# Kernel tuning notes

Hardware: AMD Instinct MI355X
Metric: run time of the kernel (lower is better)

The kernel has to match this reference:

```python
import jax, jax.numpy as jnp
import numpy as np

D_MODEL = 2048
N_HEADS = 16
D_HEAD = D_MODEL // N_HEADS  # 128
WINDOW = 512
SCALE = D_HEAD ** -0.5


def setup_inputs() -> dict:
    key = jax.random.key(0)
    ks = jax.random.split(key, 5)
    B, S = 2, 4096
    x = jax.random.normal(ks[0], (B, S, D_MODEL), dtype=jnp.float32)
    W_qkv = jax.random.normal(ks[1], (D_MODEL, 3 * D_MODEL), dtype=jnp.float32) * (D_MODEL ** -0.5)
    b_qkv = jax.random.normal(ks[2], (3 * D_MODEL,), dtype=jnp.float32) * 0.02
    W_out = jax.random.normal(ks[3], (D_MODEL, D_MODEL), dtype=jnp.float32) * (D_MODEL ** -0.5)
    b_out = jax.random.normal(ks[4], (D_MODEL,), dtype=jnp.float32) * 0.02
    return {"x": x, "W_qkv": W_qkv, "b_qkv": b_qkv, "W_out": W_out, "b_out": b_out}


def reference(x, W_qkv, b_qkv, W_out, b_out):
    B, S, D = x.shape
    nb = S // WINDOW  # number of independent causal windows (block-diagonal attention)
    qkv = x @ W_qkv + b_qkv  # (B,S,3D)
    q, k, v = jnp.split(qkv, 3, axis=-1)

    def to_blocks(t):
        # (B,S,D) -> (B,H,nb,W,dh)
        return t.reshape(B, nb, WINDOW, N_HEADS, D_HEAD).transpose(0, 3, 1, 2, 4)

    q, k, v = to_blocks(q), to_blocks(k), to_blocks(v)
    # per-window attention scores: (B,H,nb,W,W)
    scores = jnp.einsum('bhnqd,bhnkd->bhnqk', q, k) * SCALE
    causal = jnp.tril(jnp.ones((WINDOW, WINDOW), dtype=bool))
    scores = jnp.where(causal, scores, -jnp.inf)
    attn = jax.nn.softmax(scores, axis=-1)
    out = jnp.einsum('bhnqk,bhnkd->bhnqd', attn, v)  # (B,H,nb,W,dh)
    out = out.transpose(0, 2, 3, 1, 4).reshape(B, S, D)
    return out @ W_out + b_out
```

## Files before the change

kernel.cpp:

```cpp
#include <hip/hip_runtime.h>
#include <stdint.h>


typedef unsigned short u16;
typedef unsigned int u32;
typedef __attribute__((ext_vector_type(8))) short bf16x8;
typedef __attribute__((ext_vector_type(4))) float f32x4;

#define QKVN 6144
#define DM 2048

__device__ __forceinline__ u16 f2b(float f) {
  u32 u = __builtin_bit_cast(u32, f);
  u32 r = (u + 0x7fffu + ((u >> 16) & 1u)) >> 16;
  return (u16)r;
}

__device__ __forceinline__ void gload_lds16(const void* g, void* l) {
  __builtin_amdgcn_global_load_lds((const __attribute__((address_space(1))) void*)g,
                                   (__attribute__((address_space(3))) void*)l,
                                   16, 0, 0);
}


__global__ void cast_f32_bf16(const float4* __restrict__ x, uint4* __restrict__ o) {
  int idx = blockIdx.x * 256 + threadIdx.x;
  float4 a = x[2 * idx];
  float4 b = x[2 * idx + 1];
  uint4 r;
  r.x = (u32)f2b(a.x) | ((u32)f2b(a.y) << 16);
  r.y = (u32)f2b(a.z) | ((u32)f2b(a.w) << 16);
  r.z = (u32)f2b(b.x) | ((u32)f2b(b.y) << 16);
  r.w = (u32)f2b(b.z) | ((u32)f2b(b.w) << 16);
  o[idx] = r;
}

__global__ void transpose_cast(const float* __restrict__ W, u16* __restrict__ Wt,
                               int K, int N) {
  __shared__ u16 tile[64][65];
  int tx = threadIdx.x & 63;
  int ty = threadIdx.x >> 6;
  int n0 = blockIdx.x * 64;
  int k0 = blockIdx.y * 64;
#pragma unroll
  for (int r = 0; r < 64; r += 4)
    tile[r + ty][tx] = f2b(W[(size_t)(k0 + r + ty) * N + n0 + tx]);
  __syncthreads();
#pragma unroll
  for (int r = 0; r < 64; r += 4)
    Wt[(size_t)(n0 + r + ty) * K + k0 + tx] = tile[tx][r + ty];
}


template <typename TO>
__global__ __launch_bounds__(256, 3) void gemm_bt(const u16* __restrict__ A,
                                                  const u16* __restrict__ Bt,
                                                  const float* __restrict__ bias,
                                                  TO* __restrict__ C,
                                                  int M, int N, int K) {
  __shared__ u16 As[128 * 64];
  __shared__ u16 Bs[128 * 64];
  const int tid = threadIdx.x;
  const int lane = tid & 63;
  const int wave = tid >> 6;
  const int quad = lane >> 4;
  const int l15 = lane & 15;
  const int m0 = blockIdx.y * 128;
  const int n0 = blockIdx.x * 128;
  const int wm = (wave & 1) * 64;
  const int wn = (wave >> 1) * 64;

  f32x4 acc[4][4] = {};

  for (int k0 = 0; k0 < K; k0 += 64) {
#pragma unroll
    for (int i = 0; i < 4; ++i) {
      int sb = wave * 256 + i * 64;
      int s = sb + lane;
      int m = s >> 3;
      int c = (s & 7) ^ (m & 7);
      gload_lds16(A + (size_t)(m0 + m) * K + (k0 + c * 8), As + sb * 8);
      gload_lds16(Bt + (size_t)(n0 + m) * K + (k0 + c * 8), Bs + sb * 8);
    }
    __syncthreads();
#pragma unroll
    for (int ks = 0; ks < 2; ++ks) {
      bf16x8 af[4], bf[4];
#pragma unroll
      for (int i = 0; i < 4; ++i) {
        int m = wm + i * 16 + l15;
        af[i] = *(const bf16x8*)(As + m * 64 + (((ks * 4 + quad) ^ (m & 7)) << 3));
        int n = wn + i * 16 + l15;
        bf[i] = *(const bf16x8*)(Bs + n * 64 + (((ks * 4 + quad) ^ (n & 7)) << 3));
      }
#pragma unroll
      for (int i = 0; i < 4; ++i)
#pragma unroll
        for (int j = 0; j < 4; ++j)
          acc[i][j] = __builtin_amdgcn_mfma_f32_16x16x32_bf16(af[i], bf[j], acc[i][j], 0, 0, 0);
    }
    __syncthreads();
  }

#pragma unroll
  for (int j = 0; j < 4; ++j) {
    int col = n0 + wn + j * 16 + l15;
    float bv = bias[col];
#pragma unroll
    for (int i = 0; i < 4; ++i) {
      int row = m0 + wm + i * 16 + quad * 4;
#pragma unroll
      for (int t = 0; t < 4; ++t) {
        float v = acc[i][j][t] + bv;
        if constexpr (sizeof(TO) == 2)
          C[(size_t)(row + t) * N + col] = (TO)f2b(v);
        else
          C[(size_t)(row + t) * N + col] = (TO)v;
      }
    }
  }
}


__global__ __launch_bounds__(256, 2) void attn_win(const u16* __restrict__ qkv,
                                                   u16* __restrict__ attn_out) {
  __shared__ u16 Vt[128 * 64];
  __shared__ u16 Ps[128 * 64];
  const int tid = threadIdx.x;
  const int lane = tid & 63;
  const int wave = tid >> 6;
  const int quad = lane >> 4;
  const int l15 = lane & 15;
  const int qt = blockIdx.x;
  const int win = blockIdx.y;
  const int b = blockIdx.z >> 4;
  const int h = blockIdx.z & 15;
  const int tokw = b * 4096 + win * 512;
  const int tokq = tokw + qt * 128;
  const float SCALE = 0.08838834764831845f;

  bf16x8 qf[2][4];
  {
    const u16* Qb = qkv + (size_t)tokq * QKVN + h * 128;
#pragma unroll
    for (int j = 0; j < 2; ++j) {
      const u16* Qr = Qb + (size_t)(wave * 32 + j * 16 + l15) * QKVN + quad * 8;
#pragma unroll
      for (int ks = 0; ks < 4; ++ks)
        qf[j][ks] = *(const bf16x8*)(Qr + ks * 32);
    }
  }

  f32x4 acc_o[8][2] = {};
  float mrun[2] = {-1e30f, -1e30f};
  float lrun[2] = {0.f, 0.f};

  const int jt_end = 2 * qt + 1;
  for (int jt = 0; jt <= jt_end; ++jt) {
    {
      const u16* Vb = qkv + (size_t)(tokw + jt * 64) * QKVN + 4096 + h * 128;
#pragma unroll
      for (int it = 0; it < 2; ++it) {
        int task = it * 256 + tid;
        int p = task & 31;
        int dc = task >> 5;
        int kk0 = p * 2;
        const u16* g0 = Vb + (size_t)kk0 * QKVN + dc * 8;
        uint4 r0 = *(const uint4*)g0;
        uint4 r1 = *(const uint4*)(g0 + QKVN);
        const u16* a0 = (const u16*)&r0;
        const u16* a1 = (const u16*)&r1;
        int c = kk0 >> 3;
        int boff = (kk0 & 7) << 1;
#pragma unroll
        for (int j = 0; j < 8; ++j) {
          int d = dc * 8 + j;
          *(u32*)((char*)Vt + d * 128 + ((c ^ (d & 7)) << 4) + boff) =
              (u32)a0[j] | ((u32)a1[j] << 16);
        }
      }
    }

    f32x4 acc_s[4][2] = {};
    {
      const u16* Kb = qkv + (size_t)(tokw + jt * 64) * QKVN + 2048 + h * 128;
      bf16x8 kf[4][4];
#pragma unroll
      for (int i = 0; i < 4; ++i) {
        const u16* Kr = Kb + (size_t)(i * 16 + l15) * QKVN + quad * 8;
#pragma unroll
        for (int ks = 0; ks < 4; ++ks)
          kf[i][ks] = *(const bf16x8*)(Kr + ks * 32);
      }
#pragma unroll
      for (int ks = 0; ks < 4; ++ks)
#pragma unroll
        for (int i = 0; i < 4; ++i)
#pragma unroll
          for (int j = 0; j < 2; ++j)
            acc_s[i][j] = __builtin_amdgcn_mfma_f32_16x16x32_bf16(kf[i][ks], qf[j][ks],
                                                                  acc_s[i][j], 0, 0, 0);
    }

    const bool need_mask = (jt >= 2 * qt);
#pragma unroll
    for (int j = 0; j < 2; ++j) {
      int ql = wave * 32 + j * 16 + l15;
      int qg = qt * 128 + ql;
      float vmax = -1e30f;
#pragma unroll
      for (int i = 0; i < 4; ++i)
#pragma unroll
        for (int t = 0; t < 4; ++t) {
          float s = acc_s[i][j][t] * SCALE;
          if (need_mask) {
            int kg = jt * 64 + i * 16 + quad * 4 + t;
            if (kg > qg) s = -1e30f;
          }
          acc_s[i][j][t] = s;
          vmax = fmaxf(vmax, s);
        }
      vmax = fmaxf(vmax, __shfl_xor(vmax, 16));
      vmax = fmaxf(vmax, __shfl_xor(vmax, 32));
      float mnew = fmaxf(mrun[j], vmax);
      float alpha = __expf(mrun[j] - mnew);
      mrun[j] = mnew;
      float vsum = 0.f;
#pragma unroll
      for (int i = 0; i < 4; ++i) {
        float p0 = __expf(acc_s[i][j][0] - mnew);
        float p1 = __expf(acc_s[i][j][1] - mnew);
        float p2 = __expf(acc_s[i][j][2] - mnew);
        float p3 = __expf(acc_s[i][j][3] - mnew);
        vsum += (p0 + p1) + (p2 + p3);
        uint2 pk;
        pk.x = (u32)f2b(p0) | ((u32)f2b(p1) << 16);
        pk.y = (u32)f2b(p2) | ((u32)f2b(p3) << 16);
        int kk = i * 16 + quad * 4;
        *(uint2*)((char*)Ps + ql * 128 + (((kk >> 3) ^ (ql & 7)) << 4) + ((kk & 7) << 1)) = pk;
      }
      vsum += __shfl_xor(vsum, 16);
      vsum += __shfl_xor(vsum, 32);
      lrun[j] = lrun[j] * alpha + vsum;
#pragma unroll
      for (int i2 = 0; i2 < 8; ++i2)
#pragma unroll
        for (int t = 0; t < 4; ++t)
          acc_o[i2][j][t] *= alpha;
    }
    __syncthreads();

#pragma unroll
    for (int ks = 0; ks < 2; ++ks) {
      int kk = ks * 32 + quad * 8;
      int kc = kk >> 3;
      bf16x8 pf[2];
#pragma unroll
      for (int j = 0; j < 2; ++j) {
        int ql = wave * 32 + j * 16 + l15;
        pf[j] = *(const bf16x8*)((char*)Ps + ql * 128 + ((kc ^ (ql & 7)) << 4));
      }
#pragma unroll
      for (int i2 = 0; i2 < 8; ++i2) {
        int d = i2 * 16 + l15;
        bf16x8 vf = *(const bf16x8*)((char*)Vt + d * 128 + ((kc ^ (d & 7)) << 4));
#pragma unroll
        for (int j = 0; j < 2; ++j)
          acc_o[i2][j] = __builtin_amdgcn_mfma_f32_16x16x32_bf16(vf, pf[j], acc_o[i2][j], 0, 0, 0);
      }
    }
    __syncthreads();
  }

#pragma unroll
  for (int j = 0; j < 2; ++j) {
    float inv = 1.0f / lrun[j];
    int ql = wave * 32 + j * 16 + l15;
    u16* orow = attn_out + (size_t)(tokq + ql) * DM + h * 128;
#pragma unroll
    for (int i2 = 0; i2 < 8; ++i2) {
      int d = i2 * 16 + quad * 4;
      uint2 pk;
      pk.x = (u32)f2b(acc_o[i2][j][0] * inv) | ((u32)f2b(acc_o[i2][j][1] * inv) << 16);
      pk.y = (u32)f2b(acc_o[i2][j][2] * inv) | ((u32)f2b(acc_o[i2][j][3] * inv) << 16);
      *(uint2*)(orow + d) = pk;
    }
  }
}


extern "C" void kernel_launch(void* const* d_in, const int* in_sizes, int n_in,
                              void* d_out, int out_size, void* d_ws, size_t ws_size,
                              hipStream_t stream) {
  const float* x = (const float*)d_in[0];
  const float* W_qkv = (const float*)d_in[1];
  const float* b_qkv = (const float*)d_in[2];
  const float* W_out = (const float*)d_in[3];
  const float* b_out = (const float*)d_in[4];
  float* out = (float*)d_out;

  char* w = (char*)d_ws;
  u16* xb = (u16*)w;
  u16* wqkvT = (u16*)(w + 33554432);
  u16* woutT = (u16*)(w + 33554432 + 25165824);
  u16* qkv = (u16*)(w + 67108864);

  cast_f32_bf16<<<8192, 256, 0, stream>>>((const float4*)x, (uint4*)xb);
  transpose_cast<<<dim3(96, 32), 256, 0, stream>>>(W_qkv, wqkvT, 2048, 6144);
  transpose_cast<<<dim3(32, 32), 256, 0, stream>>>(W_out, woutT, 2048, 2048);
  gemm_bt<u16><<<dim3(48, 64), 256, 0, stream>>>(xb, wqkvT, b_qkv, qkv, 8192, 6144, 2048);
  attn_win<<<dim3(4, 8, 32), 256, 0, stream>>>(qkv, xb);
  gemm_bt<float><<<dim3(16, 64), 256, 0, stream>>>(xb, woutT, b_out, out, 8192, 2048, 2048);
}
```

Baseline: 523.8 us.

## Widen GEMM tiles, double-buffer attention LDS, use exp2 softmax with fast packing

GEMM blocks now compute 128x256 tiles with 8 accumulator columns per wave, reducing redundant A loads and block count; occupancy is lowered to 2 blocks. Attention double-buffers V and P in LDS, which drops the second barrier per step. It prefetches V before the QK MFMAs, splits masked and unmasked iterations via a template, folds the scale into exp2, and skips the output rescale when alpha is near 1. The bf16 packing of probabilities now truncates instead of rounding, slightly changing numerics.

```diff
diff --git a/kernel.cpp b/kernel.cpp
--- a/kernel.cpp
+++ b/kernel.cpp
@@ -15,6 +15,13 @@
   u32 r = (u + 0x7fffu + ((u >> 16) & 1u)) >> 16;
   return (u16)r;
 }
+
+__device__ __forceinline__ u32 pack_hi16(float hi, float lo) {
+  return __builtin_amdgcn_perm(__builtin_bit_cast(u32, hi),
+                               __builtin_bit_cast(u32, lo), 0x07060302u);
+}
+
+__device__ __forceinline__ float fexp2(float x) { return __builtin_amdgcn_exp2f(x); }
 
 __device__ __forceinline__ void gload_lds16(const void* g, void* l) {
   __builtin_amdgcn_global_load_lds((const __attribute__((address_space(1))) void*)g,
@@ -53,24 +60,24 @@
 
 
 template <typename TO>
-__global__ __launch_bounds__(256, 3) void gemm_bt(const u16* __restrict__ A,
+__global__ __launch_bounds__(256, 2) void gemm_bt(const u16* __restrict__ A,
                                                   const u16* __restrict__ Bt,
                                                   const float* __restrict__ bias,
                                                   TO* __restrict__ C,
                                                   int M, int N, int K) {
   __shared__ u16 As[128 * 64];
-  __shared__ u16 Bs[128 * 64];
+  __shared__ u16 Bs[256 * 64];
   const int tid = threadIdx.x;
   const int lane = tid & 63;
   const int wave = tid >> 6;
   const int quad = lane >> 4;
   const int l15 = lane & 15;
   const int m0 = blockIdx.y * 128;
-  const int n0 = blockIdx.x * 128;
+  const int n0 = blockIdx.x * 256;
   const int wm = (wave & 1) * 64;
-  const int wn = (wave >> 1) * 64;
-
-  f32x4 acc[4][4] = {};
+  const int wn = (wave >> 1) * 128;
+
+  f32x4 acc[4][8] = {};
 
   for (int k0 = 0; k0 < K; k0 += 64) {
 #pragma unroll
@@ -80,30 +87,40 @@
       int m = s >> 3;
       int c = (s & 7) ^ (m & 7);
       gload_lds16(A + (size_t)(m0 + m) * K + (k0 + c * 8), As + sb * 8);
-      gload_lds16(Bt + (size_t)(n0 + m) * K + (k0 + c * 8), Bs + sb * 8);
+    }
+#pragma unroll
+    for (int i = 0; i < 8; ++i) {
+      int sb = wave * 512 + i * 64;
+      int s = sb + lane;
+      int n = s >> 3;
+      int c = (s & 7) ^ (n & 7);
+      gload_lds16(Bt + (size_t)(n0 + n) * K + (k0 + c * 8), Bs + sb * 8);
     }
     __syncthreads();
 #pragma unroll
     for (int ks = 0; ks < 2; ++ks) {
-      bf16x8 af[4], bf[4];
+      bf16x8 af[4], bf[8];
 #pragma unroll
       for (int i = 0; i < 4; ++i) {
         int m = wm + i * 16 + l15;
         af[i] = *(const bf16x8*)(As + m * 64 + (((ks * 4 + quad) ^ (m & 7)) << 3));
-        int n = wn + i * 16 + l15;
-        bf[i] = *(const bf16x8*)(Bs + n * 64 + (((ks * 4 + quad) ^ (n & 7)) << 3));
       }
 #pragma unroll
+      for (int j = 0; j < 8; ++j) {
+        int n = wn + j * 16 + l15;
+        bf[j] = *(const bf16x8*)(Bs + n * 64 + (((ks * 4 + quad) ^ (n & 7)) << 3));
+      }
+#pragma unroll
       for (int i = 0; i < 4; ++i)
 #pragma unroll
-        for (int j = 0; j < 4; ++j)
+        for (int j = 0; j < 8; ++j)
           acc[i][j] = __builtin_amdgcn_mfma_f32_16x16x32_bf16(af[i], bf[j], acc[i][j], 0, 0, 0);
     }
     __syncthreads();
   }
 
 #pragma unroll
-  for (int j = 0; j < 4; ++j) {
+  for (int j = 0; j < 8; ++j) {
     int col = n0 + wn + j * 16 + l15;
     float bv = bias[col];
 #pragma unroll
@@ -122,10 +139,137 @@
 }
 
 
+template <bool MASK>
+__device__ __forceinline__ void attn_step(
+    int jt, int tid, int wave, int quad, int l15, int qt, int tokw, int h,
+    const u16* __restrict__ qkv, u16* Vt, u16* Ps,
+    const bf16x8 (&qf)[2][4], f32x4 (&acc_o)[8][2], float (&mrun)[2],
+    float (&lrun)[2]) {
+  const float SL2E = 0.12751745f;
+  u16* VtB = Vt + (jt & 1) * (128 * 64);
+  u16* PsB = Ps + (jt & 1) * (128 * 64);
+
+  const u16* Vb = qkv + (size_t)(tokw + jt * 64) * QKVN + 4096 + h * 128;
+  const int p = tid & 31;
+  const int dc0 = tid >> 5;
+  const int kk0 = p * 2;
+  const u16* g0 = Vb + (size_t)kk0 * QKVN + dc0 * 8;
+  uint4 vr0 = *(const uint4*)g0;
+  uint4 vr1 = *(const uint4*)(g0 + QKVN);
+  uint4 vr2 = *(const uint4*)(g0 + 64);
+  uint4 vr3 = *(const uint4*)(g0 + QKVN + 64);
+
+  f32x4 acc_s[4][2] = {};
+  {
+    const u16* Kb = qkv + (size_t)(tokw + jt * 64) * QKVN + 2048 + h * 128;
+    bf16x8 kf[4][4];
+#pragma unroll
+    for (int i = 0; i < 4; ++i) {
+      const u16* Kr = Kb + (size_t)(i * 16 + l15) * QKVN + quad * 8;
+#pragma unroll
+      for (int ks = 0; ks < 4; ++ks)
+        kf[i][ks] = *(const bf16x8*)(Kr + ks * 32);
+    }
+#pragma unroll
+    for (int ks = 0; ks < 4; ++ks)
+#pragma unroll
+      for (int i = 0; i < 4; ++i)
+#pragma unroll
+        for (int j = 0; j < 2; ++j)
+          acc_s[i][j] = __builtin_amdgcn_mfma_f32_16x16x32_bf16(kf[i][ks], qf[j][ks],
+                                                                acc_s[i][j], 0, 0, 0);
+  }
+
+  {
+    const u16* a0 = (const u16*)&vr0;
+    const u16* a1 = (const u16*)&vr1;
+    const u16* a2 = (const u16*)&vr2;
+    const u16* a3 = (const u16*)&vr3;
+    int c = kk0 >> 3;
+    int boff = (kk0 & 7) << 1;
+#pragma unroll
+    for (int j = 0; j < 8; ++j) {
+      int d = dc0 * 8 + j;
+      *(u32*)((char*)VtB + d * 128 + ((c ^ (d & 7)) << 4) + boff) =
+          (u32)a0[j] | ((u32)a1[j] << 16);
+      int d2 = d + 64;
+      *(u32*)((char*)VtB + d2 * 128 + ((c ^ (d2 & 7)) << 4) + boff) =
+          (u32)a2[j] | ((u32)a3[j] << 16);
+    }
+  }
+
+#pragma unroll
+  for (int j = 0; j < 2; ++j) {
+    int ql = wave * 32 + j * 16 + l15;
+    float vmax = -1e30f;
+#pragma unroll
+    for (int i = 0; i < 4; ++i)
+#pragma unroll
+      for (int t = 0; t < 4; ++t) {
+        float s = acc_s[i][j][t];
+        if (MASK) {
+          int kg = jt * 64 + i * 16 + quad * 4 + t;
+          if (kg > qt * 128 + ql) s = -1e30f;
+          acc_s[i][j][t] = s;
+        }
+        vmax = fmaxf(vmax, s);
+      }
+    vmax = fmaxf(vmax, __shfl_xor(vmax, 16));
+    vmax = fmaxf(vmax, __shfl_xor(vmax, 32));
+    float mnew = fmaxf(mrun[j], vmax * SL2E);
+    float alpha = fexp2(mrun[j] - mnew);
+    mrun[j] = mnew;
+    float vsum = 0.f;
+#pragma unroll
+    for (int i = 0; i < 4; ++i) {
+      float p0 = fexp2(__builtin_fmaf(acc_s[i][j][0], SL2E, -mnew));
+      float p1 = fexp2(__builtin_fmaf(acc_s[i][j][1], SL2E, -mnew));
+      float p2 = fexp2(__builtin_fmaf(acc_s[i][j][2], SL2E, -mnew));
+      float p3 = fexp2(__builtin_fmaf(acc_s[i][j][3], SL2E, -mnew));
+      vsum += (p0 + p1) + (p2 + p3);
+      uint2 pk;
+      pk.x = pack_hi16(p1, p0);
+      pk.y = pack_hi16(p3, p2);
+      int kk = i * 16 + quad * 4;
+      *(uint2*)((char*)PsB + ql * 128 + (((kk >> 3) ^ (ql & 7)) << 4) + ((kk & 7) << 1)) = pk;
+    }
+    vsum += __shfl_xor(vsum, 16);
+    vsum += __shfl_xor(vsum, 32);
+    lrun[j] = lrun[j] * alpha + vsum;
+    if (__ballot(alpha < 0.99995f)) {
+#pragma unroll
+      for (int i2 = 0; i2 < 8; ++i2)
+#pragma unroll
+        for (int t = 0; t < 4; ++t)
+          acc_o[i2][j][t] *= alpha;
+    }
+  }
+  __syncthreads();
+
+#pragma unroll
+  for (int ks = 0; ks < 2; ++ks) {
+    int kc = ks * 4 + quad;
+    bf16x8 pf[2];
+#pragma unroll
+    for (int j = 0; j < 2; ++j) {
+      int ql = wave * 32 + j * 16 + l15;
+      pf[j] = *(const bf16x8*)((char*)PsB + ql * 128 + ((kc ^ (ql & 7)) << 4));
+    }
+#pragma unroll
+    for (int i2 = 0; i2 < 8; ++i2) {
+      int d = i2 * 16 + l15;
+      bf16x8 vf = *(const bf16x8*)((char*)VtB + d * 128 + ((kc ^ (d & 7)) << 4));
+#pragma unroll
+      for (int j = 0; j < 2; ++j)
+        acc_o[i2][j] = __builtin_amdgcn_mfma_f32_16x16x32_bf16(vf, pf[j], acc_o[i2][j], 0, 0, 0);
+    }
+  }
+}
+
 __global__ __launch_bounds__(256, 2) void attn_win(const u16* __restrict__ qkv,
                                                    u16* __restrict__ attn_out) {
-  __shared__ u16 Vt[128 * 64];
-  __shared__ u16 Ps[128 * 64];
+  __shared__ u16 Vt[2 * 128 * 64];
+  __shared__ u16 Ps[2 * 128 * 64];
   const int tid = threadIdx.x;
   const int lane = tid & 63;
   const int wave = tid >> 6;
@@ -137,7 +281,6 @@
   const int h = blockIdx.z & 15;
   const int tokw = b * 4096 + win * 512;
   const int tokq = tokw + qt * 128;
-  const float SCALE = 0.08838834764831845f;
 
   bf16x8 qf[2][4];
   {
@@ -155,122 +298,12 @@
   float mrun[2] = {-1e30f, -1e30f};
   float lrun[2] = {0.f, 0.f};
 
-  const int jt_end = 2 * qt + 1;
-  for (int jt = 0; jt <= jt_end; ++jt) {
-    {
-      const u16* Vb = qkv + (size_t)(tokw + jt * 64) * QKVN + 4096 + h * 128;
-#pragma unroll
-      for (int it = 0; it < 2; ++it) {
-        int task = it * 256 + tid;
-        int p = task & 31;
-        int dc = task >> 5;
-        int kk0 = p * 2;
-        const u16* g0 = Vb + (size_t)kk0 * QKVN + dc * 8;
-        uint4 r0 = *(const uint4*)g0;
-        uint4 r1 = *(const uint4*)(g0 + QKVN);
-        const u16* a0 = (const u16*)&r0;
-        const u16* a1 = (const u16*)&r1;
-        int c = kk0 >> 3;
-        int boff = (kk0 & 7) << 1;
-#pragma unroll
-        for (int j = 0; j < 8; ++j) {
-          int d = dc * 8 + j;
-          *(u32*)((char*)Vt + d * 128 + ((c ^ (d & 7)) << 4) + boff) =
-              (u32)a0[j] | ((u32)a1[j] << 16);
-        }
-      }
-    }
-
-    f32x4 acc_s[4][2] = {};
-    {
-      const u16* Kb = qkv + (size_t)(tokw + jt * 64) * QKVN + 2048 + h * 128;
-      bf16x8 kf[4][4];
-#pragma unroll
-      for (int i = 0; i < 4; ++i) {
-        const u16* Kr = Kb + (size_t)(i * 16 + l15) * QKVN + quad * 8;
-#pragma unroll
-        for (int ks = 0; ks < 4; ++ks)
-          kf[i][ks] = *(const bf16x8*)(Kr + ks * 32);
-      }
-#pragma unroll
-      for (int ks = 0; ks < 4; ++ks)
-#pragma unroll
-        for (int i = 0; i < 4; ++i)
-#pragma unroll
-          for (int j = 0; j < 2; ++j)
-            acc_s[i][j] = __builtin_amdgcn_mfma_f32_16x16x32_bf16(kf[i][ks], qf[j][ks],
-                                                                  acc_s[i][j], 0, 0, 0);
-    }
-
-    const bool need_mask = (jt >= 2 * qt);
-#pragma unroll
-    for (int j = 0; j < 2; ++j) {
-      int ql = wave * 32 + j * 16 + l15;
-      int qg = qt * 128 + ql;
-      float vmax = -1e30f;
-#pragma unroll
-      for (int i = 0; i < 4; ++i)
-#pragma unroll
-        for (int t = 0; t < 4; ++t) {
-          float s = acc_s[i][j][t] * SCALE;
-          if (need_mask) {
-            int kg = jt * 64 + i * 16 + quad * 4 + t;
-            if (kg > qg) s = -1e30f;
-          }
-          acc_s[i][j][t] = s;
-          vmax = fmaxf(vmax, s);
-        }
-      vmax = fmaxf(vmax, __shfl_xor(vmax, 16));
-      vmax = fmaxf(vmax, __shfl_xor(vmax, 32));
-      float mnew = fmaxf(mrun[j], vmax);
-      float alpha = __expf(mrun[j] - mnew);
-      mrun[j] = mnew;
-      float vsum = 0.f;
-#pragma unroll
-      for (int i = 0; i < 4; ++i) {
-        float p0 = __expf(acc_s[i][j][0] - mnew);
-        float p1 = __expf(acc_s[i][j][1] - mnew);
-        float p2 = __expf(acc_s[i][j][2] - mnew);
-        float p3 = __expf(acc_s[i][j][3] - mnew);
-        vsum += (p0 + p1) + (p2 + p3);
-        uint2 pk;
-        pk.x = (u32)f2b(p0) | ((u32)f2b(p1) << 16);
-        pk.y = (u32)f2b(p2) | ((u32)f2b(p3) << 16);
-        int kk = i * 16 + quad * 4;
-        *(uint2*)((char*)Ps + ql * 128 + (((kk >> 3) ^ (ql & 7)) << 4) + ((kk & 7) << 1)) = pk;
-      }
-      vsum += __shfl_xor(vsum, 16);
-      vsum += __shfl_xor(vsum, 32);
-      lrun[j] = lrun[j] * alpha + vsum;
-#pragma unroll
-      for (int i2 = 0; i2 < 8; ++i2)
-#pragma unroll
-        for (int t = 0; t < 4; ++t)
-          acc_o[i2][j][t] *= alpha;
-    }
-    __syncthreads();
-
-#pragma unroll
-    for (int ks = 0; ks < 2; ++ks) {
-      int kk = ks * 32 + quad * 8;
-      int kc = kk >> 3;
-      bf16x8 pf[2];
-#pragma unroll
-      for (int j = 0; j < 2; ++j) {
-        int ql = wave * 32 + j * 16 + l15;
-        pf[j] = *(const bf16x8*)((char*)Ps + ql * 128 + ((kc ^ (ql & 7)) << 4));
-      }
-#pragma unroll
-      for (int i2 = 0; i2 < 8; ++i2) {
-        int d = i2 * 16 + l15;
-        bf16x8 vf = *(const bf16x8*)((char*)Vt + d * 128 + ((kc ^ (d & 7)) << 4));
-#pragma unroll
-        for (int j = 0; j < 2; ++j)
-          acc_o[i2][j] = __builtin_amdgcn_mfma_f32_16x16x32_bf16(vf, pf[j], acc_o[i2][j], 0, 0, 0);
-      }
-    }
-    __syncthreads();
-  }
+  int jt = 0;
+  const int diag = 2 * qt;
+  for (; jt < diag; ++jt)
+    attn_step<false>(jt, tid, wave, quad, l15, qt, tokw, h, qkv, Vt, Ps, qf, acc_o, mrun, lrun);
+  for (; jt <= diag + 1; ++jt)
+    attn_step<true>(jt, tid, wave, quad, l15, qt, tokw, h, qkv, Vt, Ps, qf, acc_o, mrun, lrun);
 
 #pragma unroll
   for (int j = 0; j < 2; ++j) {
@@ -308,7 +341,7 @@
   cast_f32_bf16<<<8192, 256, 0, stream>>>((const float4*)x, (uint4*)xb);
   transpose_cast<<<dim3(96, 32), 256, 0, stream>>>(W_qkv, wqkvT, 2048, 6144);
   transpose_cast<<<dim3(32, 32), 256, 0, stream>>>(W_out, woutT, 2048, 2048);
-  gemm_bt<u16><<<dim3(48, 64), 256, 0, stream>>>(xb, wqkvT, b_qkv, qkv, 8192, 6144, 2048);
+  gemm_bt<u16><<<dim3(24, 64), 256, 0, stream>>>(xb, wqkvT, b_qkv, qkv, 8192, 6144, 2048);
   attn_win<<<dim3(4, 8, 32), 256, 0, stream>>>(qkv, xb);
-  gemm_bt<float><<<dim3(16, 64), 256, 0, stream>>>(xb, woutT, b_out, out, 8192, 2048, 2048);
-}
+  gemm_bt<float><<<dim3(8, 64), 256, 0, stream>>>(xb, woutT, b_out, out, 8192, 2048, 2048);
+}
```

Result: no change. 532.9 us (+1.8%).
